# Optimization experiments

Hardware: AMD Instinct MI355X
Metric: run time of the kernel (lower is better)

Reference implementation:

```python
import jax, jax.numpy as jnp
import numpy as np

N = 100000      # num_nodes
E = 1600000     # num_edges (avg degree 16)
D_IN = 128
D_H = 128
D_OUT = 128


def _init_linear(key, out_dim, in_dim):
    # Kaiming-uniform-like init, bound = 1/sqrt(fan_in)
    bound = 1.0 / np.sqrt(in_dim)
    return jax.random.uniform(key, (out_dim, in_dim), jnp.float32, -bound, bound)


def setup_inputs() -> dict:
    key = jax.random.key(0)
    ks = jax.random.split(key, 12)
    x = jax.random.normal(ks[0], (N, D_IN), jnp.float32)
    edge_index = jax.random.randint(ks[1], (2, E), 0, N, jnp.int32)
    dims = [(D_H, D_IN), (D_H, D_H), (D_OUT, D_H)]
    inp = {"x": x, "edge_index": edge_index}
    for i, (do, di) in enumerate(dims):
        inp[f"Wl{i}"] = _init_linear(ks[2 + 3 * i], do, di)      # lin_l: applied to aggregated neighbors
        inp[f"bl{i}"] = jnp.zeros((do,), jnp.float32)
        inp[f"Wr{i}"] = _init_linear(ks[3 + 3 * i], do, di)      # lin_r: applied to root (self) features
    return inp


def _sage_conv(x, src, dst, Wl, bl, Wr):
    # mean aggregation of source-node features at destination nodes
    msg = x[src]                                                   # [E, d]
    agg = jax.ops.segment_sum(msg, dst, num_segments=N)            # [N, d]
    deg = jax.ops.segment_sum(jnp.ones((src.shape[0],), x.dtype), dst, num_segments=N)
    mean = agg / jnp.maximum(deg, 1.0)[:, None]
    return mean @ Wl.T + bl + x @ Wr.T


def reference(x, edge_index, Wl0, bl0, Wr0, Wl1, bl1, Wr1, Wl2, bl2, Wr2):
    src, dst = edge_index[0], edge_index[1]
    # dropout is identity in eval mode
    h = jax.nn.relu(_sage_conv(x, src, dst, Wl0, bl0, Wr0))
    h = jax.nn.relu(_sage_conv(h, src, dst, Wl1, bl1, Wr1))
    return _sage_conv(h, src, dst, Wl2, bl2, Wr2)
```

## Files before the change

### kernel.cpp

```cpp
#include <hip/hip_runtime.h>
#include <hip/hip_bf16.h>

typedef __attribute__((ext_vector_type(8))) short bf16x8;
typedef __attribute__((ext_vector_type(4))) float f32x4;
typedef __attribute__((ext_vector_type(2))) float f32x2;

#define D 128
#define BCAP 8192
#define EPB 3125
#define SBMAX 512


__global__ __launch_bounds__(256) void k_mega(
    const float* __restrict__ x,
    const float* __restrict__ w0, const float* __restrict__ w1,
    const float* __restrict__ w2, const float* __restrict__ w3,
    const float* __restrict__ w4, const float* __restrict__ w5,
    __hip_bfloat16* __restrict__ xb, __hip_bfloat16* __restrict__ wb,
    int* __restrict__ gbuf, int* __restrict__ runinfo,
    const int* __restrict__ src, const int* __restrict__ dst,
    int xquad, int e, int n, int p1b)
{
    if (blockIdx.x < p1b) {
        __shared__ int lh[512], lpre[512], pscan[256];
        __shared__ int lout[3328];
        int t = threadIdx.x;
        lh[t] = 0; lh[t + 256] = 0;
        __syncthreads();
        int lo = blockIdx.x * EPB;
        int hi = lo + EPB; if (hi > e) hi = e;
        for (int i = lo + t; i < hi; i += 256) {
            int d = dst[i]; d = ((unsigned)d < (unsigned)n) ? d : 0;
            atomicAdd(&lh[d >> 8], 1);
        }
        __syncthreads();
        int c0 = lh[2 * t], c1 = lh[2 * t + 1];
        int pair = c0 + c1;
        pscan[t] = pair;
        __syncthreads();
        for (int off = 1; off < 256; off <<= 1) {
            int v = (t >= off) ? pscan[t - off] : 0;
            __syncthreads();
            pscan[t] += v;
            __syncthreads();
        }
        int excl = pscan[t] - pair;
        lpre[2 * t] = excl;
        lpre[2 * t + 1] = excl + c0;
        runinfo[(2 * t) * SBMAX + blockIdx.x]     = (excl << 16) | c0;
        runinfo[(2 * t + 1) * SBMAX + blockIdx.x] = ((excl + c0) << 16) | c1;
        lh[2 * t] = 0; lh[2 * t + 1] = 0;
        __syncthreads();
        for (int i = lo + t; i < hi; i += 256) {
            int d = dst[i]; d = ((unsigned)d < (unsigned)n) ? d : 0;
            int s = src[i]; s = ((unsigned)s < (unsigned)n) ? s : 0;
            int b = d >> 8;
            int p = lpre[b] + atomicAdd(&lh[b], 1);
            lout[p] = s | ((d & 255) << 17);
        }
        __syncthreads();
        int cnt = hi - lo;
        for (int i = t; i < cnt; i += 256) gbuf[lo + i] = lout[i];
    } else {
        int t = (blockIdx.x - p1b) * 256 + threadIdx.x;
        if (t < xquad) {
            float4 f = ((const float4*)x)[t];
            union { int2 i2; __hip_bfloat162 h2[2]; } u;
            u.h2[0] = __float22bfloat162_rn(make_float2(f.x, f.y));
            u.h2[1] = __float22bfloat162_rn(make_float2(f.z, f.w));
            ((int2*)xb)[t] = u.i2;
        }
        if (t < 6 * 4096) {
            int wsel = t >> 12, wi = t & 4095;
            const float* wp = w0;
            if (wsel == 1) wp = w1;
            else if (wsel == 2) wp = w2;
            else if (wsel == 3) wp = w3;
            else if (wsel == 4) wp = w4;
            else if (wsel == 5) wp = w5;
            float4 f = ((const float4*)wp)[wi];
            union { int2 i2; __hip_bfloat162 h2[2]; } u;
            u.h2[0] = __float22bfloat162_rn(make_float2(f.x, f.y));
            u.h2[1] = __float22bfloat162_rn(make_float2(f.z, f.w));
            ((int2*)wb)[t] = u.i2;
        }
    }
}


__global__ __launch_bounds__(256) void k_p2(
    const int* __restrict__ gbuf, const int* __restrict__ runinfo,
    int* __restrict__ deg, int* __restrict__ offs,
    int* __restrict__ csr, int n, int p1b)
{
    __shared__ int ebuf[BCAP];
    __shared__ int out[BCAP];
    __shared__ int pscan[256];
    __shared__ int hist[256], loc[256], cur[256];
    int b = blockIdx.x, t = threadIdx.x;

    int sb0 = 2 * t, sb1 = 2 * t + 1;
    int r0 = (sb0 < p1b) ? runinfo[b * SBMAX + sb0] : 0;
    int r1 = (sb1 < p1b) ? runinfo[b * SBMAX + sb1] : 0;
    int l0 = r0 & 0xffff, l1 = r1 & 0xffff;
    int pair = l0 + l1;
    pscan[t] = pair;
    __syncthreads();
    for (int off = 1; off < 256; off <<= 1) {
        int v = (t >= off) ? pscan[t - off] : 0;
        __syncthreads();
        pscan[t] += v;
        __syncthreads();
    }
    int excl = pscan[t] - pair;
    int cnt = pscan[255];
    if (cnt > BCAP) cnt = BCAP;

    if (excl < BCAP) {
        int s0 = sb0 * EPB + (r0 >> 16);
        int lim0 = (excl + l0 <= BCAP) ? l0 : (BCAP - excl);
        for (int k = 0; k < lim0; ++k) ebuf[excl + k] = gbuf[s0 + k];
        int o1 = excl + l0;
        if (o1 < BCAP) {
            int s1 = sb1 * EPB + (r1 >> 16);
            int lim1 = (o1 + l1 <= BCAP) ? l1 : (BCAP - o1);
            for (int k = 0; k < lim1; ++k) ebuf[o1 + k] = gbuf[s1 + k];
        }
    }
    __syncthreads();

    int nodes = n - b * 256; if (nodes > 256) nodes = 256;
    hist[t] = 0;
    __syncthreads();
    for (int i = t; i < cnt; i += 256)
        atomicAdd(&hist[(ebuf[i] >> 17) & 255], 1);
    __syncthreads();
    int v = hist[t];
    loc[t] = v;
    __syncthreads();
    for (int off = 1; off < 256; off <<= 1) {
        int x = (t >= off) ? loc[t - off] : 0;
        __syncthreads();
        loc[t] += x;
        __syncthreads();
    }
    int myloc = loc[t] - v;
    cur[t] = myloc;
    if (t < nodes) { deg[b * 256 + t] = v; offs[b * 256 + t] = b * BCAP + myloc; }
    __syncthreads();
    for (int i = t; i < cnt; i += 256) {
        int ed = ebuf[i];
        int p = atomicAdd(&cur[(ed >> 17) & 255], 1);
        out[p] = ed & 0x1FFFF;
    }
    __syncthreads();
    for (int i = t; i < cnt; i += 256) csr[b * BCAP + i] = out[i];
}


__device__ __forceinline__ void acc_u32(f32x2& a, unsigned p) {
    f32x2 c;
    c.x = __uint_as_float(p << 16);
    c.y = __uint_as_float(p & 0xffff0000u);
    a += c;
}

__device__ __forceinline__ void acc_i4(f32x2* acc, int4 d) {
    acc_u32(acc[0], (unsigned)d.x);
    acc_u32(acc[1], (unsigned)d.y);
    acc_u32(acc[2], (unsigned)d.z);
    acc_u32(acc[3], (unsigned)d.w);
}

__global__ __launch_bounds__(256) void k_agg(
    const __hip_bfloat16* __restrict__ h,
    const int* __restrict__ csr,
    const int* __restrict__ offs,
    const int* __restrict__ deg,
    __hip_bfloat16* __restrict__ mean,
    int n)
{
    int node = blockIdx.x * 4 + (threadIdx.x >> 6);
    int lane = threadIdx.x & 63;
    if (node >= n) return;
    int grp = lane >> 4;
    int sub = lane & 15;
    int start = offs[node];
    int cnt = deg[node];

    f32x2 acc[4];
    #pragma unroll
    for (int k = 0; k < 4; ++k) acc[k] = (f32x2){0.f, 0.f};

    const char* hb = (const char*)h;
    unsigned suboff = (unsigned)sub * 16u;
    const int* cp = csr + start + grp;

    int i = 0;
    int bulk = cnt & ~15;

    for (; i < bulk; i += 16) {
        int s[4];
        #pragma unroll
        for (int u = 0; u < 4; ++u) s[u] = cp[i + u * 4];
        int4 d[4];
        #pragma unroll
        for (int u = 0; u < 4; ++u)
            d[u] = *(const int4*)(hb + (((unsigned)s[u] << 8) | suboff));
        #pragma unroll
        for (int u = 0; u < 4; ++u) acc_i4(acc, d[u]);
    }

    if (i < cnt) {
        int4 d[4];
        #pragma unroll
        for (int u = 0; u < 4; ++u) {
            int e = i + u * 4 + grp;
            int ec = (e < cnt) ? e : (cnt - 1);
            int s = csr[start + ec];
            d[u] = *(const int4*)(hb + (((unsigned)s << 8) | suboff));
            if (e >= cnt) d[u] = make_int4(0, 0, 0, 0);
        }
        #pragma unroll
        for (int u = 0; u < 4; ++u) acc_i4(acc, d[u]);
    }

    #pragma unroll
    for (int k = 0; k < 4; ++k) {
        acc[k].x += __shfl_xor(acc[k].x, 16);
        acc[k].y += __shfl_xor(acc[k].y, 16);
        acc[k].x += __shfl_xor(acc[k].x, 32);
        acc[k].y += __shfl_xor(acc[k].y, 32);
    }

    if (grp == 0) {
        float inv = 1.0f / fmaxf((float)cnt, 1.0f);
        union { int4 i4; __hip_bfloat162 h2[4]; } u;
        #pragma unroll
        for (int k = 0; k < 4; ++k)
            u.h2[k] = __float22bfloat162_rn(make_float2(acc[k].x * inv, acc[k].y * inv));
        *(int4*)((char*)mean + (size_t)node * 256 + suboff) = u.i4;
    }
}


__global__ __launch_bounds__(512) void k_gemm(
    const __hip_bfloat16* __restrict__ A0,
    const __hip_bfloat16* __restrict__ A1,
    const __hip_bfloat16* __restrict__ Wb,
    const float* __restrict__ bias,
    float* __restrict__ outF,
    __hip_bfloat16* __restrict__ outB,
    int n, int do_relu)
{
    __shared__ __hip_bfloat16 lW[2 * 128 * 128];

    for (int g = threadIdx.x; g < 4096; g += 512) {
        int half = g >> 11;
        int rem  = g & 2047;
        int row  = rem >> 4;
        int c    = rem & 15;
        bf16x8 v = *(const bf16x8*)(Wb + half * 16384 + row * 128 + c * 8);
        *(bf16x8*)(lW + half * 16384 + row * 128 + ((c ^ (row & 7)) * 8)) = v;
    }
    __syncthreads();

    int w = threadIdx.x >> 6;
    int lane = threadIdx.x & 63;
    int m = lane & 15;
    int q = lane >> 4;
    int base = blockIdx.x * 256 + w * 32;

    f32x4 acc[2][8];
    #pragma unroll
    for (int r = 0; r < 2; ++r)
        #pragma unroll
        for (int i = 0; i < 8; ++i) acc[r][i] = (f32x4){0.f, 0.f, 0.f, 0.f};

    const __hip_bfloat16* Aps[2] = {A0, A1};

    #pragma unroll
    for (int half = 0; half < 2; ++half) {
        const __hip_bfloat16* A = Aps[half];
        #pragma unroll
        for (int kk = 0; kk < 4; ++kk) {
            bf16x8 af[2];
            #pragma unroll
            for (int r = 0; r < 2; ++r) {
                int arow = base + r * 16 + m;
                if (arow > n - 1) arow = n - 1;
                af[r] = *(const bf16x8*)(A + (size_t)arow * D + kk * 32 + q * 8);
            }
            #pragma unroll
            for (int nt = 0; nt < 8; ++nt) {
                int row = nt * 16 + m;
                int c = (kk * 4 + q) ^ (m & 7);
                bf16x8 bf = *(const bf16x8*)(lW + half * 16384 + row * 128 + c * 8);
                #pragma unroll
                for (int r = 0; r < 2; ++r)
                    acc[r][nt] = __builtin_amdgcn_mfma_f32_16x16x32_bf16(af[r], bf, acc[r][nt], 0, 0, 0);
            }
        }
    }

    #pragma unroll
    for (int r = 0; r < 2; ++r) {
        #pragma unroll
        for (int nt = 0; nt < 8; ++nt) {
            int col = nt * 16 + m;
            float b = bias[col];
            #pragma unroll
            for (int rr = 0; rr < 4; ++rr) {
                int row = base + r * 16 + q * 4 + rr;
                if (row < n) {
                    float v = acc[r][nt][rr] + b;
                    if (do_relu) v = fmaxf(v, 0.f);
                    if (outF) outF[(size_t)row * D + col] = v;
                    else      outB[(size_t)row * D + col] = __float2bfloat16(v);
                }
            }
        }
    }
}


extern "C" void kernel_launch(void* const* d_in, const int* in_sizes, int n_in,
                              void* d_out, int out_size, void* d_ws, size_t ws_size,
                              hipStream_t stream) {
    const float* x   = (const float*)d_in[0];
    const int*   ei  = (const int*)d_in[1];
    const float* Wl0 = (const float*)d_in[2];
    const float* bl0 = (const float*)d_in[3];
    const float* Wr0 = (const float*)d_in[4];
    const float* Wl1 = (const float*)d_in[5];
    const float* bl1 = (const float*)d_in[6];
    const float* Wr1 = (const float*)d_in[7];
    const float* Wl2 = (const float*)d_in[8];
    const float* bl2 = (const float*)d_in[9];
    const float* Wr2 = (const float*)d_in[10];

    const int n = in_sizes[0] / D;
    const int e = in_sizes[1] / 2;
    const int* src = ei;
    const int* dst = ei + e;
    const int nb = (n + 255) >> 8;

    uintptr_t p = ((uintptr_t)d_ws + 255) & ~(uintptr_t)255;
    auto carve = [&](size_t bytes) {
        uintptr_t r = p;
        p = (p + bytes + 255) & ~(uintptr_t)255;
        return (void*)r;
    };
    int* deg     = (int*)carve((size_t)n * 4);
    int* offs    = (int*)carve((size_t)n * 4);
    __hip_bfloat16* mean = (__hip_bfloat16*)carve((size_t)n * D * 2);
    __hip_bfloat16* F1   = (__hip_bfloat16*)carve((size_t)n * D * 2);
    __hip_bfloat16* Wb   = (__hip_bfloat16*)carve((size_t)6 * D * D * 2);
    (void)ws_size; (void)n_in; (void)out_size;

    char* ob = (char*)d_out;
    __hip_bfloat16* h0 = (__hip_bfloat16*)ob;
    int* gbuf    = (int*)(ob + (size_t)n * D * 2);
    int* runinfo = (int*)(ob + (size_t)n * D * 2 + (size_t)e * 4);
    int* csrS    = (int*)(ob + (size_t)n * D * 2 + (size_t)e * 4 + (size_t)SBMAX * 512 * 4);

    const int xquad = n * D / 4;
    const int p1b = (e + EPB - 1) / EPB;

    const int megag = p1b + (xquad + 255) / 256;
    k_mega<<<megag, 256, 0, stream>>>(
        x, Wl0, Wr0, Wl1, Wr1, Wl2, Wr2, F1, Wb, gbuf, runinfo, src, dst,
        xquad, e, n, p1b);

    k_p2<<<nb, 256, 0, stream>>>(gbuf, runinfo, deg, offs, csrS, n, p1b);

    const int ag = (n + 3) / 4;
    const int gg = (n + 255) / 256;

    __hip_bfloat16* Wb0 = Wb + 0 * 2 * D * D;
    __hip_bfloat16* Wb1 = Wb + 1 * 2 * D * D;
    __hip_bfloat16* Wb2 = Wb + 2 * 2 * D * D;

    k_agg<<<ag, 256, 0, stream>>>(F1, csrS, offs, deg, mean, n);
    k_gemm<<<gg, 512, 0, stream>>>(mean, F1, Wb0, bl0, nullptr, h0, n, 1);
    k_agg<<<ag, 256, 0, stream>>>(h0, csrS, offs, deg, mean, n);
    k_gemm<<<gg, 512, 0, stream>>>(mean, h0, Wb1, bl1, nullptr, F1, n, 1);
    k_agg<<<ag, 256, 0, stream>>>(F1, csrS, offs, deg, mean, n);
    k_gemm<<<gg, 512, 0, stream>>>(mean, F1, Wb2, bl2, (float*)d_out, nullptr, n, 0);
}
```

Before: 373.2 us.

## Pad CSR segments to multiples of 16 with a zero sentinel row, pack node descriptors

Each node's CSR segment is padded to a multiple of 16 entries, and the padding points to an extra all-zero feature row at index n. The aggregation kernel can then drop its masked tail iteration and run only the uniform 16-wide loop. Offset and degree are packed into one int2 so each node reads a single descriptor. In exchange the gather does extra loads of the zero row (an average of about 7.5 per node), and padded segments can exceed the per-bucket capacity, which the new code clamps.

After: 370.7 us. Within noise of the previous version (-0.7%).

```diff
diff --git a/kernel.cpp b/kernel.cpp
--- a/kernel.cpp
+++ b/kernel.cpp
@@ -17,6 +17,7 @@
     const float* __restrict__ w2, const float* __restrict__ w3,
     const float* __restrict__ w4, const float* __restrict__ w5,
     __hip_bfloat16* __restrict__ xb, __hip_bfloat16* __restrict__ wb,
+    __hip_bfloat16* __restrict__ h0,
     int* __restrict__ gbuf, int* __restrict__ runinfo,
     const int* __restrict__ src, const int* __restrict__ dst,
     int xquad, int e, int n, int p1b)
@@ -84,13 +85,17 @@
             u.h2[1] = __float22bfloat162_rn(make_float2(f.z, f.w));
             ((int2*)wb)[t] = u.i2;
         }
+        if (t < 16) {
+            ((int4*)(xb + (size_t)n * D))[t] = make_int4(0, 0, 0, 0);
+            ((int4*)(h0 + (size_t)n * D))[t] = make_int4(0, 0, 0, 0);
+        }
     }
 }
 
 
 __global__ __launch_bounds__(256) void k_p2(
     const int* __restrict__ gbuf, const int* __restrict__ runinfo,
-    int* __restrict__ deg, int* __restrict__ offs,
+    int2* __restrict__ ndesc,
     int* __restrict__ csr, int n, int p1b)
 {
     __shared__ int ebuf[BCAP];
@@ -136,7 +141,8 @@
         atomicAdd(&hist[(ebuf[i] >> 17) & 255], 1);
     __syncthreads();
     int v = hist[t];
-    loc[t] = v;
+    int pv = (v + 15) & ~15;
+    loc[t] = pv;
     __syncthreads();
     for (int off = 1; off < 256; off <<= 1) {
         int x = (t >= off) ? loc[t - off] : 0;
@@ -144,17 +150,21 @@
         loc[t] += x;
         __syncthreads();
     }
-    int myloc = loc[t] - v;
+    int myloc = loc[t] - pv;
+    int ptot = loc[255];
+    if (ptot > BCAP) ptot = BCAP;
     cur[t] = myloc;
-    if (t < nodes) { deg[b * 256 + t] = v; offs[b * 256 + t] = b * BCAP + myloc; }
+    if (t < nodes) ndesc[b * 256 + t] = make_int2(b * BCAP + myloc, v);
+    __syncthreads();
+    for (int i = t; i < ptot; i += 256) out[i] = n;
     __syncthreads();
     for (int i = t; i < cnt; i += 256) {
         int ed = ebuf[i];
         int p = atomicAdd(&cur[(ed >> 17) & 255], 1);
-        out[p] = ed & 0x1FFFF;
-    }
-    __syncthreads();
-    for (int i = t; i < cnt; i += 256) csr[b * BCAP + i] = out[i];
+        if (p < BCAP) out[p] = ed & 0x1FFFF;
+    }
+    __syncthreads();
+    for (int i = t; i < ptot; i += 256) csr[b * BCAP + i] = out[i];
 }
 
 
@@ -175,8 +185,7 @@
 __global__ __launch_bounds__(256) void k_agg(
     const __hip_bfloat16* __restrict__ h,
     const int* __restrict__ csr,
-    const int* __restrict__ offs,
-    const int* __restrict__ deg,
+    const int2* __restrict__ ndesc,
     __hip_bfloat16* __restrict__ mean,
     int n)
 {
@@ -185,8 +194,9 @@
     if (node >= n) return;
     int grp = lane >> 4;
     int sub = lane & 15;
-    int start = offs[node];
-    int cnt = deg[node];
+    int2 nd = ndesc[node];
+    int start = nd.x, cnt = nd.y;
+    int cntp = (cnt + 15) & ~15;
 
     f32x2 acc[4];
     #pragma unroll
@@ -196,10 +206,7 @@
     unsigned suboff = (unsigned)sub * 16u;
     const int* cp = csr + start + grp;
 
-    int i = 0;
-    int bulk = cnt & ~15;
-
-    for (; i < bulk; i += 16) {
+    for (int i = 0; i < cntp; i += 16) {
         int s[4];
         #pragma unroll
         for (int u = 0; u < 4; ++u) s[u] = cp[i + u * 4];
@@ -207,20 +214,6 @@
         #pragma unroll
         for (int u = 0; u < 4; ++u)
             d[u] = *(const int4*)(hb + (((unsigned)s[u] << 8) | suboff));
-        #pragma unroll
-        for (int u = 0; u < 4; ++u) acc_i4(acc, d[u]);
-    }
-
-    if (i < cnt) {
-        int4 d[4];
-        #pragma unroll
-        for (int u = 0; u < 4; ++u) {
-            int e = i + u * 4 + grp;
-            int ec = (e < cnt) ? e : (cnt - 1);
-            int s = csr[start + ec];
-            d[u] = *(const int4*)(hb + (((unsigned)s << 8) | suboff));
-            if (e >= cnt) d[u] = make_int4(0, 0, 0, 0);
-        }
         #pragma unroll
         for (int u = 0; u < 4; ++u) acc_i4(acc, d[u]);
     }
@@ -351,28 +344,28 @@
         p = (p + bytes + 255) & ~(uintptr_t)255;
         return (void*)r;
     };
-    int* deg     = (int*)carve((size_t)n * 4);
-    int* offs    = (int*)carve((size_t)n * 4);
+    int2* ndesc  = (int2*)carve((size_t)n * 8);
     __hip_bfloat16* mean = (__hip_bfloat16*)carve((size_t)n * D * 2);
-    __hip_bfloat16* F1   = (__hip_bfloat16*)carve((size_t)n * D * 2);
+    __hip_bfloat16* F1   = (__hip_bfloat16*)carve((size_t)(n + 1) * D * 2);
     __hip_bfloat16* Wb   = (__hip_bfloat16*)carve((size_t)6 * D * D * 2);
     (void)ws_size; (void)n_in; (void)out_size;
 
     char* ob = (char*)d_out;
     __hip_bfloat16* h0 = (__hip_bfloat16*)ob;
-    int* gbuf    = (int*)(ob + (size_t)n * D * 2);
-    int* runinfo = (int*)(ob + (size_t)n * D * 2 + (size_t)e * 4);
-    int* csrS    = (int*)(ob + (size_t)n * D * 2 + (size_t)e * 4 + (size_t)SBMAX * 512 * 4);
+    size_t hbytes = (size_t)(n + 1) * D * 2;
+    int* gbuf    = (int*)(ob + hbytes);
+    int* runinfo = (int*)(ob + hbytes + (size_t)e * 4);
+    int* csrS    = (int*)(ob + hbytes + (size_t)e * 4 + (size_t)SBMAX * 512 * 4);
 
     const int xquad = n * D / 4;
     const int p1b = (e + EPB - 1) / EPB;
 
     const int megag = p1b + (xquad + 255) / 256;
     k_mega<<<megag, 256, 0, stream>>>(
-        x, Wl0, Wr0, Wl1, Wr1, Wl2, Wr2, F1, Wb, gbuf, runinfo, src, dst,
+        x, Wl0, Wr0, Wl1, Wr1, Wl2, Wr2, F1, Wb, h0, gbuf, runinfo, src, dst,
         xquad, e, n, p1b);
 
-    k_p2<<<nb, 256, 0, stream>>>(gbuf, runinfo, deg, offs, csrS, n, p1b);
+    k_p2<<<nb, 256, 0, stream>>>(gbuf, runinfo, ndesc, csrS, n, p1b);
 
     const int ag = (n + 3) / 4;
     const int gg = (n + 255) / 256;
@@ -381,10 +374,10 @@
     __hip_bfloat16* Wb1 = Wb + 1 * 2 * D * D;
     __hip_bfloat16* Wb2 = Wb + 2 * 2 * D * D;
 
-    k_agg<<<ag, 256, 0, stream>>>(F1, csrS, offs, deg, mean, n);
+    k_agg<<<ag, 256, 0, stream>>>(F1, csrS, ndesc, mean, n);
     k_gemm<<<gg, 512, 0, stream>>>(mean, F1, Wb0, bl0, nullptr, h0, n, 1);
-    k_agg<<<ag, 256, 0, stream>>>(h0, csrS, offs, deg, mean, n);
+    k_agg<<<ag, 256, 0, stream>>>(h0, csrS, ndesc, mean, n);
     k_gemm<<<gg, 512, 0, stream>>>(mean, h0, Wb1, bl1, nullptr, F1, n, 1);
-    k_agg<<<ag, 256, 0, stream>>>(F1, csrS, offs, deg, mean, n);
+    k_agg<<<ag, 256, 0, stream>>>(F1, csrS, ndesc, mean, n);
     k_gemm<<<gg, 512, 0, stream>>>(mean, F1, Wb2, bl2, (float*)d_out, nullptr, n, 0);
 }
```
